# Kernel tuning notes

Measured on AMD Instinct MI355X. Metric: run time of the kernel, lower is better.

The kernel has to match this reference:

```python
import jax, jax.numpy as jnp
import numpy as np

B, T, DIM = 2, 2048, 1040
H = 16
HD = (DIM - 1) // H  # 64 spatial dims per head; per-head width = HD + 1
EPS = 1e-6


def _rotary_tables(seq_len, dtype):
    inv_freq = 1.0 / (10000.0 ** (jnp.arange(0, HD, 2, dtype=jnp.float32) / (HD - 2 * EPS)))
    t = jnp.arange(seq_len, dtype=jnp.float32)
    freqs = jnp.outer(t, inv_freq)  # [T, HD//2]
    cos = jnp.cos(freqs).astype(dtype)[None, :, None, :]  # [1,T,1,HD//2]
    sin = jnp.sin(freqs).astype(dtype)[None, :, None, :]
    return cos, sin


def _apply_hyp_rotary(x, cos, sin):
    # x: [B,T,H,HD+1]; component 0 is the Lorentz time coordinate
    x_sp = x[..., 1:]
    d = x_sp.shape[-1] // 2
    x1, x2 = x_sp[..., :d], x_sp[..., d:]
    y1 = x1 * cos + x2 * sin
    y2 = -x1 * sin + x2 * cos
    rot = jnp.clip(jnp.concatenate([y1, y2], axis=-1), -1000.0, 1000.0)
    sp_sq = jnp.clip(jnp.sum(rot * rot, axis=-1, keepdims=True), 0.0, 1e6)
    new_x0 = jnp.sqrt(1.0 + sp_sq + EPS)  # re-project onto hyperboloid
    return jnp.concatenate([new_x0, rot], axis=-1)


def setup_inputs() -> dict:
    key = jax.random.key(0)
    kx, kq, kk, kv, kp = jax.random.split(key, 5)
    scale = 0.02  # xavier_normal gain 0.02 in the original
    x = jax.random.normal(kx, (B, T, DIM), dtype=jnp.float32)
    Wq = jax.random.normal(kq, (DIM, DIM), dtype=jnp.float32) * scale
    Wk = jax.random.normal(kk, (DIM, DIM), dtype=jnp.float32) * scale
    Wv = jax.random.normal(kv, (DIM, DIM), dtype=jnp.float32) * scale
    Wp = jax.random.normal(kp, (DIM, DIM), dtype=jnp.float32) * scale
    return {"x": x, "Wq": Wq, "Wk": Wk, "Wv": Wv, "Wp": Wp}


def reference(x, Wq, Wk, Wv, Wp):
    b, t, _ = x.shape
    q = (x @ Wq.T).reshape(b, t, H, HD + 1)
    k = (x @ Wk.T).reshape(b, t, H, HD + 1)
    v = (x @ Wv.T).reshape(b, t, H, HD + 1)
    cos, sin = _rotary_tables(t, x.dtype)
    q = _apply_hyp_rotary(q, cos, sin)
    k = _apply_hyp_rotary(k, cos, sin)
    # Lorentzian inner product scores: -q0*k0 + <q_sp, k_sp>
    spatial = jnp.einsum('bthd,bshd->bhts', q[..., 1:], k[..., 1:])
    lorentz = jnp.einsum('bth,bsh->bhts', q[..., 0], k[..., 0])
    logits = jnp.clip((spatial - lorentz) / (HD ** 0.5), -100.0, 100.0)
    attn = jax.nn.softmax(logits, axis=-1)
    y = jnp.einsum('bhts,bshd->bthd', attn, v).reshape(b, t, DIM)
    return y @ Wp.T
```

## Files before the change

### kernel.cpp

```cpp
#include <hip/hip_runtime.h>
#include <math.h>

#define B_   2
#define T_   2048
#define DIM_ 1040
#define H_   16
#define HD_  64
#define HD1_ 65
#define NELEM (B_*T_*DIM_)

#define KP_   1056
#define NP_   1152
#define NP3_  3456
#define SEGS_ 132
#define MROWS_ (B_*T_)

#define NBH_  (B_*H_)
#define VTR_  72
#define QKW_  96

#define PR_A_ (NP3_*SEGS_)
#define PR_B_ (PR_A_ + MROWS_*SEGS_)
#define PR_C_ (PR_B_ + NBH_*7*256)
#define PR_D_ (PR_C_ + NP_*SEGS_)

typedef __attribute__((ext_vector_type(8))) __bf16 bf16x8;
typedef __attribute__((ext_vector_type(4))) float f32x4;
typedef __attribute__((ext_vector_type(8))) unsigned short ushort8;

static __device__ __forceinline__ unsigned pack_bf16(float lo, float hi) {
    __bf16 a = (__bf16)lo, c = (__bf16)hi;
    unsigned short ua, uc;
    __builtin_memcpy(&ua, &a, 2);
    __builtin_memcpy(&uc, &c, 2);
    return ((unsigned)uc << 16) | ua;
}

static __device__ __forceinline__ float exp2_fast(float x) {
    float r;
    asm("v_exp_f32 %0, %1" : "=v"(r) : "v"(x));
    return r;
}

static __device__ __forceinline__ void conv_row_plain(
    const float* __restrict__ in, __bf16* __restrict__ out, int r, int s,
    int rows_in)
{
    float v[8];
    if (r < rows_in && s < 130) {
        const float4 f0 = *(const float4*)(in + (size_t)r * DIM_ + s * 8);
        const float4 f1 = *(const float4*)(in + (size_t)r * DIM_ + s * 8 + 4);
        v[0]=f0.x; v[1]=f0.y; v[2]=f0.z; v[3]=f0.w;
        v[4]=f1.x; v[5]=f1.y; v[6]=f1.z; v[7]=f1.w;
    } else {
        #pragma unroll
        for (int i = 0; i < 8; ++i) v[i] = 0.0f;
    }
    __bf16 t[8] __attribute__((aligned(16)));
    #pragma unroll
    for (int i = 0; i < 8; ++i) t[i] = (__bf16)v[i];
    *(ushort8*)(out) = *(const ushort8*)(t);
}

__global__ __launch_bounds__(256)
void prep_all(const float* __restrict__ x,  const float* __restrict__ Wq,
              const float* __restrict__ Wk, const float* __restrict__ Wv,
              const float* __restrict__ Wp, __bf16* __restrict__ xb,
              __bf16* __restrict__ Wb3, __bf16* __restrict__ VT,
              __bf16* __restrict__ WpB)
{
    const int gid = blockIdx.x * 256 + threadIdx.x;
    if (gid < PR_A_) {
        const int r = gid / SEGS_, s = gid - r * SEGS_;
        const int seg = r / NP_, rr = r - seg * NP_;
        const float* in = (seg == 0) ? Wq : (seg == 1) ? Wk : Wv;
        conv_row_plain(in, Wb3 + (size_t)r * KP_ + s * 8, rr, s, DIM_);
    } else if (gid < PR_B_) {
        const int g = gid - PR_A_;
        const int r = g / SEGS_, s = g - r * SEGS_;
        conv_row_plain(x, xb + (size_t)r * KP_ + s * 8, r, s, MROWS_);
    } else if (gid < PR_C_) {
        const int cid = gid - PR_B_;
        const int bh  = cid / 1792;
        const int rem = cid - bh * 1792;
        const int row = 65 + rem / 256;
        const int tc  = rem - (row - 65) * 256;
        const unsigned val = (row == 65) ? 0x3F803F80u : 0u;
        unsigned* p = (unsigned*)(VT + ((size_t)bh * VTR_ + row) * T_ + tc * 8);
        p[0] = val; p[1] = val; p[2] = val; p[3] = val;
    } else {
        const int g = gid - PR_C_;
        const int r = g / SEGS_, s = g - r * SEGS_;
        conv_row_plain(Wp, WpB + (size_t)r * KP_ + s * 8, r, s, DIM_);
    }
}

__device__ __forceinline__ void gload_lds16(const void* g, void* l) {
    __builtin_amdgcn_global_load_lds(
        (const __attribute__((address_space(1))) void*)g,
        (__attribute__((address_space(3))) void*)l, 16, 0, 0);
}

#define GEMM_PURE_CORE(Ac_, Bw_, N0_, M0_)                                    \
    __shared__ __bf16 As[128 * 96];                                           \
    __shared__ __bf16 Bs[128 * 96];                                           \
    const int tid  = threadIdx.x;                                             \
    const int lane = tid & 63;                                                \
    const int w    = tid >> 6;                                                \
    const int wr   = (w >> 1) * 64, wc = (w & 1) * 64;                        \
    const __bf16* gap[6]; const __bf16* gb[6];                                \
    _Pragma("unroll")                                                         \
    for (int qi = 0; qi < 6; ++qi) {                                          \
        const int cid = qi * 256 + tid;                                       \
        const int rr  = cid / 12, cc = cid - rr * 12;                         \
        gap[qi] = Ac_ + (size_t)(M0_ + rr) * KP_ + cc * 8;                    \
        gb[qi]  = Bw_ + (size_t)(N0_ + rr) * KP_ + cc * 8;                    \
    }                                                                         \
    f32x4 acc[4][4];                                                          \
    _Pragma("unroll")                                                         \
    for (int i = 0; i < 4; ++i)                                               \
        _Pragma("unroll")                                                     \
        for (int j = 0; j < 4; ++j) acc[i][j] = (f32x4){0.f, 0.f, 0.f, 0.f};  \
    const __bf16* pa = As + (wr + (lane & 15)) * 96 + (lane >> 4) * 8;        \
    const __bf16* pb = Bs + (wc + (lane & 15)) * 96 + (lane >> 4) * 8;        \
    for (int k0 = 0; k0 < KP_; k0 += 96) {                                    \
        __syncthreads();                                                      \
        _Pragma("unroll")                                                     \
        for (int qi = 0; qi < 6; ++qi) {                                      \
            gload_lds16(gap[qi] + k0, As + (qi * 256 + tid) * 8);             \
            gload_lds16(gb[qi]  + k0, Bs + (qi * 256 + tid) * 8);             \
        }                                                                     \
        __syncthreads();                                                      \
        _Pragma("unroll")                                                     \
        for (int ks = 0; ks < 3; ++ks) {                                      \
            bf16x8 a[4], b[4];                                                \
            _Pragma("unroll")                                                 \
            for (int i = 0; i < 4; ++i)                                       \
                a[i] = *(const bf16x8*)(pa + i * 16 * 96 + ks * 32);          \
            _Pragma("unroll")                                                 \
            for (int j = 0; j < 4; ++j)                                       \
                b[j] = *(const bf16x8*)(pb + j * 16 * 96 + ks * 32);          \
            __builtin_amdgcn_s_setprio(1);                                    \
            _Pragma("unroll")                                                 \
            for (int i = 0; i < 4; ++i)                                       \
                _Pragma("unroll")                                             \
                for (int j = 0; j < 4; ++j)                                   \
                    acc[i][j] = __builtin_amdgcn_mfma_f32_16x16x32_bf16(      \
                        a[i], b[j], acc[i][j], 0, 0, 0);                      \
            __builtin_amdgcn_s_setprio(0);                                    \
        }                                                                     \
    }

__global__ __launch_bounds__(256)
void gemm_qkv_b(const __bf16* __restrict__ Ac, const __bf16* __restrict__ Bw,
                __bf16* __restrict__ Cq, __bf16* __restrict__ Ck,
                __bf16* __restrict__ VTout)
{
    const int bid = blockIdx.x;
    const int gid = (bid & 7) * 108 + (bid >> 3);
    const int n0  = (gid >> 5) * 128;
    const int m0  = (gid & 31) * 128;
    GEMM_PURE_CORE(Ac, Bw, n0, m0)

    const int seg = n0 / NP_;
    const int rbase = m0 + wr + (lane >> 4) * 4;
    const int cbase = n0 - seg * NP_ + wc + (lane & 15);

    if (seg < 2) {
        __bf16* C = seg ? Ck : Cq;
        #pragma unroll
        for (int i = 0; i < 4; ++i)
            #pragma unroll
            for (int j = 0; j < 4; ++j) {
                const int n = cbase + j * 16;
                if (n < DIM_) {
                    #pragma unroll
                    for (int r = 0; r < 4; ++r)
                        C[(size_t)(rbase + i * 16 + r) * DIM_ + n] =
                            (__bf16)acc[i][j][r];
                }
            }
    } else {
        #pragma unroll
        for (int i = 0; i < 4; ++i) {
            const int tg = rbase + i * 16;
            const int bb = tg >> 11, tt = tg & (T_ - 1);
            #pragma unroll
            for (int j = 0; j < 4; ++j) {
                const int n = cbase + j * 16;
                if (n < DIM_) {
                    const int h = n / 65, d = n - h * 65;
                    const size_t off =
                        ((size_t)(bb * H_ + h) * VTR_ + d) * T_ + tt;
                    uint2 pk;
                    pk.x = pack_bf16(acc[i][j][0], acc[i][j][1]);
                    pk.y = pack_bf16(acc[i][j][2], acc[i][j][3]);
                    *(uint2*)(VTout + off) = pk;
                }
            }
        }
    }
}

__global__ __launch_bounds__(256)
void gemm_out_b(const __bf16* __restrict__ Ac, const __bf16* __restrict__ Bw,
                float* __restrict__ C)
{
    const int bid = blockIdx.x;
    const int gid = (bid & 7) * 36 + (bid >> 3);
    const int n0  = (gid >> 5) * 128;
    const int m0  = (gid & 31) * 128;
    GEMM_PURE_CORE(Ac, Bw, n0, m0)

    const int rbase = m0 + wr + (lane >> 4) * 4;
    const int cbase = n0 + wc + (lane & 15);
    #pragma unroll
    for (int i = 0; i < 4; ++i)
        #pragma unroll
        for (int j = 0; j < 4; ++j) {
            const int n = cbase + j * 16;
            if (n < DIM_) {
                #pragma unroll
                for (int r = 0; r < 4; ++r)
                    C[(size_t)(rbase + i * 16 + r) * DIM_ + n] = acc[i][j][r];
            }
        }
}

__global__ __launch_bounds__(256)
void rotary2(const __bf16* __restrict__ Xq, const __bf16* __restrict__ Xk,
             __bf16* __restrict__ QB, __bf16* __restrict__ KB)
{
    const int gwid = (blockIdx.x * 256 + threadIdx.x) >> 6;
    const int lane = threadIdx.x & 63;
    const int which = gwid >> 16;
    const int wid   = gwid & 65535;

    const float SCALE = 0.18033688f;

    const int h  = wid & (H_ - 1);
    const int bt = wid >> 4;
    const int t  = bt & (T_ - 1);
    const int b  = bt >> 11;
    const __bf16* base = (which ? Xk : Xq) + (size_t)bt * DIM_ + h * HD1_;

    const int j = lane & 31;
    const float pw = powf(10000.0f, (float)j * (1.0f / 32.0f));
    const float fr = (float)t * (1.0f / pw);
    const float cs = cosf(fr);
    const float sn = sinf(fr);

    const float x1 = (float)base[1 + j];
    const float x2 = (float)base[33 + j];

    float rot = (lane < 32) ? (x1 * cs + x2 * sn)
                            : (x2 * cs - x1 * sn);
    rot = fminf(fmaxf(rot, -1000.0f), 1000.0f);

    float sq = rot * rot;
    #pragma unroll
    for (int off = 32; off >= 1; off >>= 1)
        sq += __shfl_xor(sq, off, 64);
    sq = fminf(fmaxf(sq, 0.0f), 1.0e6f);

    const float x0 = sqrtf((1.0f + sq) + 1.0e-6f);

    __bf16* XB = which ? KB : QB;
    const size_t base96 = (size_t)((b * H_ + h) * T_ + t) * QKW_;
    XB[base96 + lane] = which ? (__bf16)rot : (__bf16)(SCALE * rot);

    if (lane < 32) {
        float v = 0.0f;
        const float d0 = x0 - 5.25f;
        if (which) {
            const float bh = (float)(__bf16)d0;
            if (lane == 0 || lane == 2) v = bh;
            else if (lane == 1) v = d0 - bh;
        } else {
            if (lane < 2) v = -SCALE * 5.25f;
            else if (lane == 2) v = -SCALE * (float)(__bf16)d0;
        }
        XB[base96 + 64 + lane] = (__bf16)v;
    }
}

__global__ __launch_bounds__(256)
void attn_mfma7(const __bf16* __restrict__ QB, const __bf16* __restrict__ KB,
                const __bf16* __restrict__ VT, __bf16* __restrict__ yb)
{
    __shared__ __bf16 Kt[2][64 * 96] __attribute__((aligned(16)));
    __shared__ __bf16 Vt[80 * 64] __attribute__((aligned(16)));
    __shared__ __bf16 Pt[64 * 72] __attribute__((aligned(16)));

    const int tid  = threadIdx.x;
    const int lane = tid & 63;
    const int w    = tid >> 6;
    const int lx   = lane & 15;
    const int ly   = lane >> 4;
    const int bh   = blockIdx.x;
    const int q0r  = blockIdx.y * 64;

    const __bf16* QBb = QB + (size_t)bh * T_ * QKW_;
    const __bf16* KBb = KB + (size_t)bh * T_ * QKW_;
    const __bf16* VTb = VT + (size_t)bh * VTR_ * T_;

    bf16x8 aq[3];
    #pragma unroll
    for (int ks = 0; ks < 3; ++ks)
        aq[ks] = *(const bf16x8*)
            (QBb + (size_t)(q0r + w * 16 + lx) * QKW_ + ks * 32 + ly * 8);

    ((unsigned*)Vt)[2304 + tid] = 0u;

    int offk[3];
    #pragma unroll
    for (int qi = 0; qi < 3; ++qi) {
        const int cid = qi * 256 + tid;
        const int s = cid / 12, p = cid - s * 12;
        const int c = (p & 12) | ((p - (s >> 1)) & 3);
        offk[qi] = s * QKW_ + c * 8;
    }
    int offv[3];
    #pragma unroll
    for (int qi = 0; qi < 3; ++qi) {
        const int cid = qi * 256 + tid;
        const int d = cid >> 3, jj = cid & 7;
        offv[qi] = d * T_ + (jj ^ (d & 7)) * 8;
    }

    #pragma unroll
    for (int qi = 0; qi < 3; ++qi)
        gload_lds16(KBb + offk[qi], &Kt[0][(qi * 256 + tid) * 8]);

    f32x4 acc_o[5];
    #pragma unroll
    for (int n = 0; n < 5; ++n) acc_o[n] = (f32x4){0.f, 0.f, 0.f, 0.f};

    const int rr = (ly + (lx >> 1)) & 3;

    int cur = 0;
    for (int it = 0; it < T_ / 64; ++it) {
        const int s0 = it * 64;
        __syncthreads();

        gload_lds16(VTb + s0 + offv[0], Vt + tid * 8);
        gload_lds16(VTb + s0 + offv[1], Vt + (256 + tid) * 8);
        if (tid < 64)
            gload_lds16(VTb + s0 + offv[2], Vt + (512 + tid) * 8);

        if (it + 1 < T_ / 64) {
            const size_t koff = (size_t)(s0 + 64) * QKW_;
            #pragma unroll
            for (int qi = 0; qi < 3; ++qi)
                gload_lds16(KBb + koff + offk[qi],
                            &Kt[cur ^ 1][(qi * 256 + tid) * 8]);
        }

        f32x4 sc[4];
        __builtin_amdgcn_s_setprio(1);
        #pragma unroll
        for (int n = 0; n < 4; ++n) {
            f32x4 c = (f32x4){0.f, 0.f, 0.f, 0.f};
            #pragma unroll
            for (int ks = 0; ks < 3; ++ks) {
                const bf16x8 bk = *(const bf16x8*)
                    &Kt[cur][(n * 16 + lx) * 96 + ks * 32 + rr * 8];
                c = __builtin_amdgcn_mfma_f32_16x16x32_bf16(
                    aq[ks], bk, c, 0, 0, 0);
            }
            sc[n] = c;
        }
        __builtin_amdgcn_s_setprio(0);

        #pragma unroll
        for (int n = 0; n < 4; ++n)
            #pragma unroll
            for (int r = 0; r < 4; ++r)
                Pt[(w * 16 + ly * 4 + r) * 72 + n * 16 + lx] =
                    (__bf16)exp2_fast(sc[n][r]);

        __syncthreads();

        bf16x8 ap[2];
        #pragma unroll
        for (int ks = 0; ks < 2; ++ks)
            ap[ks] = *(const bf16x8*)
                &Pt[(w * 16 + lx) * 72 + ks * 32 + ly * 8];
        __builtin_amdgcn_s_setprio(1);
        #pragma unroll
        for (int n = 0; n < 5; ++n) {
            f32x4 c = acc_o[n];
            #pragma unroll
            for (int ks = 0; ks < 2; ++ks) {
                const bf16x8 bv = *(const bf16x8*)
                    &Vt[(n * 16 + lx) * 64 + ((ks * 4 + ly) ^ (lx & 7)) * 8];
                c = __builtin_amdgcn_mfma_f32_16x16x32_bf16(
                    ap[ks], bv, c, 0, 0, 0);
            }
            acc_o[n] = c;
        }
        __builtin_amdgcn_s_setprio(0);
        cur ^= 1;
    }

    const int b = bh >> 4, h = bh & 15;
    #pragma unroll
    for (int r = 0; r < 4; ++r) {
        const float l = __shfl(acc_o[4][r], (lane & 48) + 1, 64);
        const float inv = 1.0f / l;
        const int qrow = q0r + w * 16 + ly * 4 + r;
        __bf16* yrow = yb + (size_t)(b * T_ + qrow) * KP_ + h * HD1_;
        #pragma unroll
        for (int n = 0; n < 4; ++n)
            yrow[n * 16 + lx] = (__bf16)(acc_o[n][r] * inv);
        if (lx == 0) yrow[64] = (__bf16)(acc_o[4][r] * inv);
    }
}

extern "C" void kernel_launch(void* const* d_in, const int* in_sizes, int n_in,
                              void* d_out, int out_size, void* d_ws, size_t ws_size,
                              hipStream_t stream)
{
    const float* x  = (const float*)d_in[0];
    const float* Wq = (const float*)d_in[1];
    const float* Wk = (const float*)d_in[2];
    const float* Wv = (const float*)d_in[3];
    const float* Wp = (const float*)d_in[4];

    __bf16* qb  = (__bf16*)d_ws;
    __bf16* kb  = qb + (size_t)MROWS_ * DIM_;
    __bf16* xb  = kb + (size_t)MROWS_ * DIM_;
    __bf16* Wb3 = xb + (size_t)MROWS_ * KP_;
    __bf16* QB  = Wb3 + (size_t)NP3_ * KP_;
    __bf16* KB  = QB + (size_t)NBH_ * T_ * QKW_;
    __bf16* VT  = KB + (size_t)NBH_ * T_ * QKW_;
    __bf16* WpB = VT + (size_t)NBH_ * VTR_ * T_;
    __bf16* yb  = xb;

    float* out = (float*)d_out;

    dim3 blk(256);

    prep_all<<<dim3(PR_D_ / 256), blk, 0, stream>>>(
        x, Wq, Wk, Wv, Wp, xb, Wb3, VT, WpB);
    gemm_qkv_b<<<dim3(864), blk, 0, stream>>>(xb, Wb3, qb, kb, VT);

    rotary2<<<dim3(2 * (B_ * T_ * H_) / 4), blk, 0, stream>>>(qb, kb, QB, KB);

    attn_mfma7<<<dim3(NBH_, T_ / 64), blk, 0, stream>>>(QB, KB, VT, yb);

    gemm_out_b<<<dim3(288), blk, 0, stream>>>(yb, WpB, out);
}
```

Baseline: 228.3 us.

## Process 128 query rows per attention block to reuse K/V tiles

Each attention workgroup now handles two 64-row query tiles instead of one. Every K and V tile loaded into LDS feeds twice as many MFMAs, which halves global K/V traffic and the per-tile sync overhead. In exchange the grid drops from 1024 to 512 blocks, and register and LDS use per block go up (a larger P buffer plus doubled accumulators), which may lower occupancy.

Measured after the change: 210.5 us, median of 2. 7.8% less time.

```diff
diff --git a/kernel.cpp b/kernel.cpp
--- a/kernel.cpp
+++ b/kernel.cpp
@@ -285,12 +285,12 @@
 }
 
 __global__ __launch_bounds__(256)
-void attn_mfma7(const __bf16* __restrict__ QB, const __bf16* __restrict__ KB,
+void attn_mfma9(const __bf16* __restrict__ QB, const __bf16* __restrict__ KB,
                 const __bf16* __restrict__ VT, __bf16* __restrict__ yb)
 {
     __shared__ __bf16 Kt[2][64 * 96] __attribute__((aligned(16)));
     __shared__ __bf16 Vt[80 * 64] __attribute__((aligned(16)));
-    __shared__ __bf16 Pt[64 * 72] __attribute__((aligned(16)));
+    __shared__ __bf16 Pt[128 * 72] __attribute__((aligned(16)));
 
     const int tid  = threadIdx.x;
     const int lane = tid & 63;
@@ -298,17 +298,20 @@
     const int lx   = lane & 15;
     const int ly   = lane >> 4;
     const int bh   = blockIdx.x;
-    const int q0r  = blockIdx.y * 64;
+    const int q0r  = blockIdx.y * 128;
 
     const __bf16* QBb = QB + (size_t)bh * T_ * QKW_;
     const __bf16* KBb = KB + (size_t)bh * T_ * QKW_;
     const __bf16* VTb = VT + (size_t)bh * VTR_ * T_;
 
-    bf16x8 aq[3];
-    #pragma unroll
-    for (int ks = 0; ks < 3; ++ks)
-        aq[ks] = *(const bf16x8*)
-            (QBb + (size_t)(q0r + w * 16 + lx) * QKW_ + ks * 32 + ly * 8);
+    bf16x8 aq[2][3];
+    #pragma unroll
+    for (int t = 0; t < 2; ++t)
+        #pragma unroll
+        for (int ks = 0; ks < 3; ++ks)
+            aq[t][ks] = *(const bf16x8*)
+                (QBb + (size_t)(q0r + t * 64 + w * 16 + lx) * QKW_ +
+                 ks * 32 + ly * 8);
 
     ((unsigned*)Vt)[2304 + tid] = 0u;
 
@@ -332,9 +335,11 @@
     for (int qi = 0; qi < 3; ++qi)
         gload_lds16(KBb + offk[qi], &Kt[0][(qi * 256 + tid) * 8]);
 
-    f32x4 acc_o[5];
-    #pragma unroll
-    for (int n = 0; n < 5; ++n) acc_o[n] = (f32x4){0.f, 0.f, 0.f, 0.f};
+    f32x4 acc_o[2][5];
+    #pragma unroll
+    for (int t = 0; t < 2; ++t)
+        #pragma unroll
+        for (int n = 0; n < 5; ++n) acc_o[t][n] = (f32x4){0.f, 0.f, 0.f, 0.f};
 
     const int rr = (ly + (lx >> 1)) & 3;
 
@@ -356,65 +361,74 @@
                             &Kt[cur ^ 1][(qi * 256 + tid) * 8]);
         }
 
-        f32x4 sc[4];
-        __builtin_amdgcn_s_setprio(1);
-        #pragma unroll
-        for (int n = 0; n < 4; ++n) {
-            f32x4 c = (f32x4){0.f, 0.f, 0.f, 0.f};
-            #pragma unroll
-            for (int ks = 0; ks < 3; ++ks) {
-                const bf16x8 bk = *(const bf16x8*)
-                    &Kt[cur][(n * 16 + lx) * 96 + ks * 32 + rr * 8];
-                c = __builtin_amdgcn_mfma_f32_16x16x32_bf16(
-                    aq[ks], bk, c, 0, 0, 0);
+        #pragma unroll
+        for (int t = 0; t < 2; ++t) {
+            f32x4 sc[4];
+            __builtin_amdgcn_s_setprio(1);
+            #pragma unroll
+            for (int n = 0; n < 4; ++n) {
+                f32x4 c = (f32x4){0.f, 0.f, 0.f, 0.f};
+                #pragma unroll
+                for (int ks = 0; ks < 3; ++ks) {
+                    const bf16x8 bk = *(const bf16x8*)
+                        &Kt[cur][(n * 16 + lx) * 96 + ks * 32 + rr * 8];
+                    c = __builtin_amdgcn_mfma_f32_16x16x32_bf16(
+                        aq[t][ks], bk, c, 0, 0, 0);
+                }
+                sc[n] = c;
             }
-            sc[n] = c;
-        }
-        __builtin_amdgcn_s_setprio(0);
-
-        #pragma unroll
-        for (int n = 0; n < 4; ++n)
-            #pragma unroll
-            for (int r = 0; r < 4; ++r)
-                Pt[(w * 16 + ly * 4 + r) * 72 + n * 16 + lx] =
-                    (__bf16)exp2_fast(sc[n][r]);
+            __builtin_amdgcn_s_setprio(0);
+
+            #pragma unroll
+            for (int n = 0; n < 4; ++n)
+                #pragma unroll
+                for (int r = 0; r < 4; ++r)
+                    Pt[(t * 64 + w * 16 + ly * 4 + r) * 72 + n * 16 + lx] =
+                        (__bf16)exp2_fast(sc[n][r]);
+        }
 
         __syncthreads();
 
-        bf16x8 ap[2];
-        #pragma unroll
-        for (int ks = 0; ks < 2; ++ks)
-            ap[ks] = *(const bf16x8*)
-                &Pt[(w * 16 + lx) * 72 + ks * 32 + ly * 8];
-        __builtin_amdgcn_s_setprio(1);
-        #pragma unroll
-        for (int n = 0; n < 5; ++n) {
-            f32x4 c = acc_o[n];
-            #pragma unroll
-            for (int ks = 0; ks < 2; ++ks) {
-                const bf16x8 bv = *(const bf16x8*)
-                    &Vt[(n * 16 + lx) * 64 + ((ks * 4 + ly) ^ (lx & 7)) * 8];
-                c = __builtin_amdgcn_mfma_f32_16x16x32_bf16(
-                    ap[ks], bv, c, 0, 0, 0);
+        #pragma unroll
+        for (int t = 0; t < 2; ++t) {
+            bf16x8 ap[2];
+            #pragma unroll
+            for (int ks = 0; ks < 2; ++ks)
+                ap[ks] = *(const bf16x8*)
+                    &Pt[(t * 64 + w * 16 + lx) * 72 + ks * 32 + ly * 8];
+            __builtin_amdgcn_s_setprio(1);
+            #pragma unroll
+            for (int n = 0; n < 5; ++n) {
+                f32x4 c = acc_o[t][n];
+                #pragma unroll
+                for (int ks = 0; ks < 2; ++ks) {
+                    const bf16x8 bv = *(const bf16x8*)
+                        &Vt[(n * 16 + lx) * 64 +
+                            ((ks * 4 + ly) ^ (lx & 7)) * 8];
+                    c = __builtin_amdgcn_mfma_f32_16x16x32_bf16(
+                        ap[ks], bv, c, 0, 0, 0);
+                }
+                acc_o[t][n] = c;
             }
-            acc_o[n] = c;
-        }
-        __builtin_amdgcn_s_setprio(0);
+            __builtin_amdgcn_s_setprio(0);
+        }
         cur ^= 1;
     }
 
     const int b = bh >> 4, h = bh & 15;
     #pragma unroll
-    for (int r = 0; r < 4; ++r) {
-        const float l = __shfl(acc_o[4][r], (lane & 48) + 1, 64);
-        const float inv = 1.0f / l;
-        const int qrow = q0r + w * 16 + ly * 4 + r;
-        __bf16* yrow = yb + (size_t)(b * T_ + qrow) * KP_ + h * HD1_;
-        #pragma unroll
-        for (int n = 0; n < 4; ++n)
-            yrow[n * 16 + lx] = (__bf16)(acc_o[n][r] * inv);
-        if (lx == 0) yrow[64] = (__bf16)(acc_o[4][r] * inv);
-    }
+    for (int t = 0; t < 2; ++t)
+        #pragma unroll
+        for (int r = 0; r < 4; ++r) {
+            const float l = __shfl(acc_o[t][4][r], (lane & 48) + 1, 64);
+            const float inv = 1.0f / l;
+            const int qrow = q0r + t * 64 + w * 16 + ly * 4 + r;
+            __bf16* yrow = yb + (size_t)(b * T_ + qrow) * KP_ + h * HD1_;
+            #pragma unroll
+            for (int n = 0; n < 4; ++n)
+                yrow[n * 16 + lx] = (__bf16)(acc_o[t][n][r] * inv);
+            if (lx == 0) yrow[64] = (__bf16)(acc_o[t][4][r] * inv);
+        }
 }
 
 extern "C" void kernel_launch(void* const* d_in, const int* in_sizes, int n_in,
@@ -447,7 +461,7 @@
 
     rotary2<<<dim3(2 * (B_ * T_ * H_) / 4), blk, 0, stream>>>(qb, kb, QB, KB);
 
-    attn_mfma7<<<dim3(NBH_, T_ / 64), blk, 0, stream>>>(QB, KB, VT, yb);
+    attn_mfma9<<<dim3(NBH_, T_ / 128), blk, 0, stream>>>(QB, KB, VT, yb);
 
     gemm_out_b<<<dim3(288), blk, 0, stream>>>(yb, WpB, out);
 }
```
